# Kernel tuning notes

Hardware: AMD Instinct MI355X
Metric: run time of the kernel (lower is better)

## Reference

```python
import jax, jax.numpy as jnp
import numpy as np
from jax import lax

B, CIN, COUT, H, W, WDIM, K = 8, 256, 256, 64, 64, 512, 3
EPS = 1e-8
LRELU_SLOPE = 0.2


def setup_inputs() -> dict:
    key = jax.random.key(0)
    k_x, k_w, k_n, k_sw, k_cw = jax.random.split(key, 5)
    x = jax.random.normal(k_x, (B, CIN, H, W), dtype=jnp.float32)
    w = jax.random.normal(k_w, (B, WDIM), dtype=jnp.float32)
    noise = jax.random.normal(k_n, (B, 1, H, W), dtype=jnp.float32)
    # Equalized-LR params: stored ~N(0,1), scaled at use-time by 1/sqrt(fan_in)
    style_weight = jax.random.normal(k_sw, (CIN, WDIM), dtype=jnp.float32)
    style_bias = jnp.ones((CIN,), dtype=jnp.float32)  # StyleGAN style bias init = 1
    conv_weight = jax.random.normal(k_cw, (COUT, CIN, K, K), dtype=jnp.float32)
    noise_weight = jnp.zeros((COUT,), dtype=jnp.float32)  # NoiseInjection per-channel scale
    bias = jnp.zeros((COUT,), dtype=jnp.float32)
    return {"x": x, "w": w, "noise": noise, "style_weight": style_weight,
            "style_bias": style_bias, "conv_weight": conv_weight,
            "noise_weight": noise_weight, "bias": bias}


def reference(x, w, noise, style_weight, style_bias, conv_weight, noise_weight, bias):
    # EqualizedLinear: s = w @ (W * 1/sqrt(w_dim))^T + b  -> [B, CIN]
    s = jnp.einsum("bd,cd->bc", w, style_weight) * (1.0 / np.sqrt(WDIM)) + style_bias
    # Equalized conv weight scale
    wk = conv_weight * (1.0 / np.sqrt(CIN * K * K))  # [COUT, CIN, K, K]
    # Demodulation coefficient per (sample, out-channel):
    # demod = rsqrt(sum_{cin,kh,kw} (wk * s)^2 + eps)
    w2 = jnp.einsum("oikl,oikl->oi", wk, wk)               # [COUT, CIN]
    demod = lax.rsqrt(jnp.einsum("oi,bi->bo", w2, s * s) + EPS)  # [B, COUT]
    # Equivalent fused form: scale input per-channel, one shared conv, scale output
    xm = x * s[:, :, None, None]
    y = lax.conv_general_dilated(
        xm, wk, window_strides=(1, 1), padding="SAME",
        dimension_numbers=("NCHW", "OIHW", "NCHW"))
    y = y * demod[:, :, None, None]
    # NoiseInjection + bias + LeakyReLU(0.2)
    y = y + noise_weight[None, :, None, None] * noise + bias[None, :, None, None]
    return jnp.where(y >= 0, y, LRELU_SLOPE * y)
```

## Files before the change

### kernel.cpp

```cpp
#include <hip/hip_runtime.h>
#include <hip/hip_bf16.h>


typedef __attribute__((ext_vector_type(8))) short bf16x8;
typedef __attribute__((ext_vector_type(4))) float f32x4;

#define INV_SQRT_WDIM 0.04419417382415922f

__global__ __launch_bounds__(256)
void style_kernel(const float* __restrict__ w, const float* __restrict__ sw,
                  const float* __restrict__ sb, float* __restrict__ s) {
  const int b = blockIdx.x;
  const int c = threadIdx.x;
  float acc = 0.f;
#pragma unroll 8
  for (int d = 0; d < 512; ++d) acc += w[b * 512 + d] * sw[c * 512 + d];
  s[b * 256 + c] = acc * INV_SQRT_WDIM + sb[c];
}

__global__ __launch_bounds__(256)
void demod_kernel(const float* __restrict__ cw, const float* __restrict__ s,
                  float* __restrict__ demod) {
  const int o = blockIdx.x;
  const int i = threadIdx.x;
  float w2 = 0.f;
#pragma unroll
  for (int t = 0; t < 9; ++t) {
    float v = cw[(o * 256 + i) * 9 + t];
    w2 += v * v;
  }
  __shared__ float red[4];
  for (int b = 0; b < 8; ++b) {
    float sv = s[b * 256 + i];
    float val = w2 * sv * sv;
#pragma unroll
    for (int off = 32; off > 0; off >>= 1) val += __shfl_down(val, off);
    if ((i & 63) == 0) red[i >> 6] = val;
    __syncthreads();
    if (i == 0) {
      float tot = red[0] + red[1] + red[2] + red[3];
      demod[b * 256 + o] = rsqrtf(tot * (1.0f / 2304.0f) + 1e-8f);
    }
    __syncthreads();
  }
}

__global__ __launch_bounds__(256)
void wtrans_kernel(const float* __restrict__ cw, __hip_bfloat16* __restrict__ wt) {
  const int e = blockIdx.x * 256 + threadIdx.x;
  const int tap = e >> 16;
  const int o = (e >> 8) & 255;
  const int i = e & 255;
  wt[e] = __float2bfloat16(cw[(o * 256 + i) * 9 + tap] * (1.0f / 48.0f));
}

__global__ __launch_bounds__(256)
void xmod_kernel(const float* __restrict__ x, const float* __restrict__ s,
                 __hip_bfloat16* __restrict__ xt) {
  const int h = blockIdx.x;
  const int b = blockIdx.y;
  __shared__ __hip_bfloat16 tile[256 * 66];
  const int t = threadIdx.x;
  const int wl4 = (t & 15) * 4;
#pragma unroll 4
  for (int p = 0; p < 16; ++p) {
    const int i = p * 16 + (t >> 4);
    const float4 v = *(const float4*)&x[((b * 256 + i) * 64 + h) * 64 + wl4];
    const float sv = s[b * 256 + i];
    const int wsw = wl4 ^ (((i >> 3) & 7) << 3);
    unsigned lo = ((unsigned)__bfloat16_as_ushort(__float2bfloat16(v.y * sv)) << 16) |
                  (unsigned)__bfloat16_as_ushort(__float2bfloat16(v.x * sv));
    unsigned hi = ((unsigned)__bfloat16_as_ushort(__float2bfloat16(v.w * sv)) << 16) |
                  (unsigned)__bfloat16_as_ushort(__float2bfloat16(v.z * sv));
    *(unsigned*)&tile[i * 66 + wsw] = lo;
    *(unsigned*)&tile[i * 66 + wsw + 2] = hi;
  }
  __syncthreads();
#pragma unroll 2
  for (int p = 0; p < 8; ++p) {
    const int w = p * 8 + (t >> 5);
    const int c = t & 31;
    ushort out8[8];
#pragma unroll
    for (int j = 0; j < 8; ++j) {
      const int i = c * 8 + j;
      const int wsw = w ^ (((i >> 3) & 7) << 3);
      out8[j] = __bfloat16_as_ushort(tile[i * 66 + wsw]);
    }
    *(uint4*)&xt[((b * 64 + h) * 64 + w) * 256 + c * 8] = *(uint4*)out8;
  }
}

__global__ __launch_bounds__(256, 2)
void conv_mfma_kernel(const __hip_bfloat16* __restrict__ xt,
                      const __hip_bfloat16* __restrict__ wt,
                      const float* __restrict__ demod,
                      const float* __restrict__ noise,
                      const float* __restrict__ nw,
                      const float* __restrict__ bias,
                      float* __restrict__ out) {
  __shared__ __hip_bfloat16 xlds[6 * 64 * 32] __attribute__((aligned(16)));
  __shared__ __hip_bfloat16 wlds[9 * 64 * 32] __attribute__((aligned(16)));

  const int tid = threadIdx.x;
  const int lane = tid & 63;
  const int wv = tid >> 6;

  const int h0 = blockIdx.x * 4;
  const int oc0 = blockIdx.y * 64;
  const int b = blockIdx.z;

  const int abase = (lane & 15) * 32 + 8 * (lane >> 4);

  int boff[4][3];
  bool bok[4][3];
#pragma unroll
  for (int q = 0; q < 4; ++q)
#pragma unroll
    for (int tj = 0; tj < 3; ++tj) {
      int wx = q * 16 + (lane & 15) + tj - 1;
      bool ok = (unsigned)wx < 64u;
      int wc = ok ? wx : 0;
      boff[q][tj] = wc * 32 + 8 * (lane >> 4);
      bok[q][tj] = ok;
    }

  const f32x4 zero4 = {0.f, 0.f, 0.f, 0.f};
  const bf16x8 zerov = {0, 0, 0, 0, 0, 0, 0, 0};
  f32x4 acc[4][4];
#pragma unroll
  for (int m = 0; m < 4; ++m)
#pragma unroll
    for (int q = 0; q < 4; ++q) acc[m][q] = zero4;

  for (int cc = 0; cc < 8; ++cc) {
    const int c0 = cc * 32;
    __syncthreads();

#pragma unroll
    for (int k = 0; k < 6; ++k) {
      const int gX = tid + k * 256;
      const int r = gX >> 8;
      const int w = (gX >> 2) & 63;
      const int g = gX & 3;
      const int gr = h0 - 1 + r;
      uint4 v = make_uint4(0u, 0u, 0u, 0u);
      if ((unsigned)gr < 64u)
        v = *(const uint4*)&xt[((b * 64 + gr) * 64 + w) * 256 + c0 + 8 * g];
      *(uint4*)&xlds[gX * 8] = v;
    }
#pragma unroll
    for (int k = 0; k < 9; ++k) {
      const int gW = tid + k * 256;
      const int t9 = gW >> 8;
      const int o = (gW >> 2) & 63;
      const int g = gW & 3;
      uint4 v = *(const uint4*)&wt[t9 * 65536 + (oc0 + o) * 256 + c0 + 8 * g];
      *(uint4*)&wlds[gW * 8] = v;
    }
    __syncthreads();

#pragma unroll
    for (int ti = 0; ti < 3; ++ti) {
#pragma unroll
      for (int tj = 0; tj < 3; ++tj) {
        const int t = ti * 3 + tj;
        bf16x8 av[4];
#pragma unroll
        for (int m = 0; m < 4; ++m)
          av[m] = *(const bf16x8*)&wlds[t * 2048 + m * 512 + abase];
#pragma unroll
        for (int q = 0; q < 4; ++q) {
          bf16x8 bv = *(const bf16x8*)&xlds[(wv + ti) * 2048 + boff[q][tj]];
          if (!bok[q][tj]) bv = zerov;
#pragma unroll
          for (int m = 0; m < 4; ++m)
            acc[m][q] = __builtin_amdgcn_mfma_f32_16x16x32_bf16(av[m], bv, acc[m][q], 0, 0, 0);
        }
      }
    }
  }

  const int hrow = h0 + wv;
  float nzv[4];
#pragma unroll
  for (int q = 0; q < 4; ++q)
    nzv[q] = noise[b * 4096 + hrow * 64 + q * 16 + (lane & 15)];
#pragma unroll
  for (int m = 0; m < 4; ++m) {
#pragma unroll
    for (int reg = 0; reg < 4; ++reg) {
      const int oc = oc0 + m * 16 + (lane >> 4) * 4 + reg;
      const float dm = demod[b * 256 + oc];
      const float nwv = nw[oc];
      const float bvv = bias[oc];
#pragma unroll
      for (int q = 0; q < 4; ++q) {
        float v = acc[m][q][reg] * dm + nwv * nzv[q] + bvv;
        v = (v >= 0.f) ? v : 0.2f * v;
        out[((b * 256 + oc) * 64 + hrow) * 64 + q * 16 + (lane & 15)] = v;
      }
    }
  }
}

extern "C" void kernel_launch(void* const* d_in, const int* in_sizes, int n_in,
                              void* d_out, int out_size, void* d_ws, size_t ws_size,
                              hipStream_t stream) {
  const float* x     = (const float*)d_in[0];
  const float* w     = (const float*)d_in[1];
  const float* noise = (const float*)d_in[2];
  const float* sw    = (const float*)d_in[3];
  const float* sb    = (const float*)d_in[4];
  const float* cw    = (const float*)d_in[5];
  const float* nw    = (const float*)d_in[6];
  const float* bias  = (const float*)d_in[7];
  float* out = (float*)d_out;

  char* ws = (char*)d_ws;
  float* s            = (float*)(ws);
  float* demod        = (float*)(ws + 8192);
  __hip_bfloat16* wt  = (__hip_bfloat16*)(ws + 16384);
  __hip_bfloat16* xt  = (__hip_bfloat16*)(ws + 1196032);

  style_kernel<<<8, 256, 0, stream>>>(w, sw, sb, s);
  demod_kernel<<<256, 256, 0, stream>>>(cw, s, demod);
  wtrans_kernel<<<2304, 256, 0, stream>>>(cw, wt);
  xmod_kernel<<<dim3(64, 8), 256, 0, stream>>>(x, s, xt);
  conv_mfma_kernel<<<dim3(16, 4, 8), 256, 0, stream>>>(
      xt, wt, demod, noise, nw, bias, out);
}
```

Before: 163.3 us.

## Double-buffer input tiles via direct-to-LDS loads, read weights from global, fuse prep kernels

The conv kernel now stages the modulated input tile straight into LDS with global_load_lds, double-buffered so the next channel chunk loads while the current one computes. Weights are no longer staged in LDS. They are pre-laid out in MFMA fragment order and read directly from global, which frees LDS so occupancy can go to 3 blocks per SM. The style GEMV is parallelised over channels, and the demod and weight-transpose kernels are merged into one. The input layout gets an XOR slot swizzle, and a zero buffer covers out-of-range rows. The risks are higher latency from global weight reads inside the MFMA loop and register pressure at the new launch bound.

```diff
diff --git a/kernel.cpp b/kernel.cpp
--- a/kernel.cpp
+++ b/kernel.cpp
@@ -7,51 +7,75 @@
 
 #define INV_SQRT_WDIM 0.04419417382415922f
 
+__device__ __forceinline__ void gload_lds16(const void* g, void* l) {
+  __builtin_amdgcn_global_load_lds(
+      (const __attribute__((address_space(1))) void*)g,
+      (__attribute__((address_space(3))) void*)l, 16, 0, 0);
+}
+
 __global__ __launch_bounds__(256)
-void style_kernel(const float* __restrict__ w, const float* __restrict__ sw,
-                  const float* __restrict__ sb, float* __restrict__ s) {
-  const int b = blockIdx.x;
-  const int c = threadIdx.x;
-  float acc = 0.f;
-#pragma unroll 8
-  for (int d = 0; d < 512; ++d) acc += w[b * 512 + d] * sw[c * 512 + d];
-  s[b * 256 + c] = acc * INV_SQRT_WDIM + sb[c];
+void style2_kernel(const float* __restrict__ w, const float* __restrict__ sw,
+                   const float* __restrict__ sb, float* __restrict__ s) {
+  const int c = blockIdx.x, t = threadIdx.x;
+  const int lane = t & 63, wvi = t >> 6;
+  const float2 swv = *(const float2*)&sw[c * 512 + t * 2];
+  __shared__ float red[4][8];
+  float acc[8];
+#pragma unroll
+  for (int b = 0; b < 8; ++b) {
+    const float2 wv2 = *(const float2*)&w[b * 512 + t * 2];
+    acc[b] = swv.x * wv2.x + swv.y * wv2.y;
+  }
+#pragma unroll
+  for (int b = 0; b < 8; ++b)
+#pragma unroll
+    for (int off = 32; off > 0; off >>= 1) acc[b] += __shfl_down(acc[b], off);
+  if (lane == 0)
+#pragma unroll
+    for (int b = 0; b < 8; ++b) red[wvi][b] = acc[b];
+  __syncthreads();
+  if (t < 8) {
+    float tot = red[0][t] + red[1][t] + red[2][t] + red[3][t];
+    s[t * 256 + c] = tot * INV_SQRT_WDIM + sb[c];
+  }
 }
 
 __global__ __launch_bounds__(256)
-void demod_kernel(const float* __restrict__ cw, const float* __restrict__ s,
-                  float* __restrict__ demod) {
-  const int o = blockIdx.x;
-  const int i = threadIdx.x;
+void wdm_kernel(const float* __restrict__ cw, const float* __restrict__ s,
+                __hip_bfloat16* __restrict__ wt2, float* __restrict__ demod) {
+  const int o = blockIdx.x, i = threadIdx.x;
+  const int lane = i & 63, wvi = i >> 6;
+  float v[9];
   float w2 = 0.f;
 #pragma unroll
   for (int t = 0; t < 9; ++t) {
-    float v = cw[(o * 256 + i) * 9 + t];
-    w2 += v * v;
-  }
-  __shared__ float red[4];
+    v[t] = cw[(o * 256 + i) * 9 + t];
+    w2 += v[t] * v[t];
+  }
+  const int wbase = (i >> 5) * 8192 + (o >> 4) * 512 + ((i >> 3) & 3) * 128 +
+                    (o & 15) * 8 + (i & 7);
+#pragma unroll
+  for (int t = 0; t < 9; ++t)
+    wt2[t * 65536 + wbase] = __float2bfloat16(v[t] * (1.0f / 48.0f));
+  __shared__ float red[4][8];
+  float pv[8];
+#pragma unroll
   for (int b = 0; b < 8; ++b) {
-    float sv = s[b * 256 + i];
-    float val = w2 * sv * sv;
-#pragma unroll
-    for (int off = 32; off > 0; off >>= 1) val += __shfl_down(val, off);
-    if ((i & 63) == 0) red[i >> 6] = val;
-    __syncthreads();
-    if (i == 0) {
-      float tot = red[0] + red[1] + red[2] + red[3];
-      demod[b * 256 + o] = rsqrtf(tot * (1.0f / 2304.0f) + 1e-8f);
-    }
-    __syncthreads();
-  }
-}
-
-__global__ __launch_bounds__(256)
-void wtrans_kernel(const float* __restrict__ cw, __hip_bfloat16* __restrict__ wt) {
-  const int e = blockIdx.x * 256 + threadIdx.x;
-  const int tap = e >> 16;
-  const int o = (e >> 8) & 255;
-  const int i = e & 255;
-  wt[e] = __float2bfloat16(cw[(o * 256 + i) * 9 + tap] * (1.0f / 48.0f));
+    const float sv = s[b * 256 + i];
+    pv[b] = w2 * sv * sv;
+  }
+#pragma unroll
+  for (int b = 0; b < 8; ++b)
+#pragma unroll
+    for (int off = 32; off > 0; off >>= 1) pv[b] += __shfl_down(pv[b], off);
+  if (lane == 0)
+#pragma unroll
+    for (int b = 0; b < 8; ++b) red[wvi][b] = pv[b];
+  __syncthreads();
+  if (i < 8) {
+    float tot = red[0][i] + red[1][i] + red[2][i] + red[3][i];
+    demod[i * 256 + o] = rsqrtf(tot * (1.0f / 2304.0f) + 1e-8f);
+  }
 }
 
 __global__ __launch_bounds__(256)
@@ -87,20 +111,22 @@
       const int wsw = w ^ (((i >> 3) & 7) << 3);
       out8[j] = __bfloat16_as_ushort(tile[i * 66 + wsw]);
     }
-    *(uint4*)&xt[((b * 64 + h) * 64 + w) * 256 + c * 8] = *(uint4*)out8;
-  }
-}
-
-__global__ __launch_bounds__(256, 2)
+    const int slot = (c & 3) ^ ((w >> 1) & 3);
+    *(uint4*)&xt[((b * 64 + h) * 64 + w) * 256 + (c >> 2) * 32 + slot * 8] =
+        *(uint4*)out8;
+  }
+}
+
+__global__ __launch_bounds__(256, 3)
 void conv_mfma_kernel(const __hip_bfloat16* __restrict__ xt,
-                      const __hip_bfloat16* __restrict__ wt,
+                      const __hip_bfloat16* __restrict__ wt2,
                       const float* __restrict__ demod,
                       const float* __restrict__ noise,
                       const float* __restrict__ nw,
                       const float* __restrict__ bias,
+                      const __hip_bfloat16* __restrict__ zbuf,
                       float* __restrict__ out) {
-  __shared__ __hip_bfloat16 xlds[6 * 64 * 32] __attribute__((aligned(16)));
-  __shared__ __hip_bfloat16 wlds[9 * 64 * 32] __attribute__((aligned(16)));
+  __shared__ __hip_bfloat16 xlds[2][12288] __attribute__((aligned(16)));
 
   const int tid = threadIdx.x;
   const int lane = tid & 63;
@@ -110,7 +136,8 @@
   const int oc0 = blockIdx.y * 64;
   const int b = blockIdx.z;
 
-  const int abase = (lane & 15) * 32 + 8 * (lane >> 4);
+  const int aoff = (lane >> 4) * 128 + (lane & 15) * 8;
+  const int o16b = oc0 >> 4;
 
   int boff[4][3];
   bool bok[4][3];
@@ -121,7 +148,8 @@
       int wx = q * 16 + (lane & 15) + tj - 1;
       bool ok = (unsigned)wx < 64u;
       int wc = ok ? wx : 0;
-      boff[q][tj] = wc * 32 + 8 * (lane >> 4);
+      int slot = (lane >> 4) ^ ((wc >> 1) & 3);
+      boff[q][tj] = wc * 32 + slot * 8;
       bok[q][tj] = ok;
     }
 
@@ -133,33 +161,28 @@
 #pragma unroll
     for (int q = 0; q < 4; ++q) acc[m][q] = zero4;
 
+  auto stage = [&](int buf, int scc) {
+#pragma unroll
+    for (int k = 0; k < 6; ++k) {
+      const int ch = wv * 6 + k;
+      const int r = ch >> 2;
+      const int wseg = ch & 3;
+      const int gr = h0 - 1 + r;
+      const __hip_bfloat16* src =
+          ((unsigned)gr < 64u)
+              ? xt + ((b * 64 + gr) * 64 + wseg * 16 + (lane >> 2)) * 256 +
+                    scc * 32 + (lane & 3) * 8
+              : zbuf;
+      gload_lds16(src, &xlds[buf][ch * 512]);
+    }
+  };
+
+  stage(0, 0);
+  __syncthreads();
+
   for (int cc = 0; cc < 8; ++cc) {
-    const int c0 = cc * 32;
-    __syncthreads();
-
-#pragma unroll
-    for (int k = 0; k < 6; ++k) {
-      const int gX = tid + k * 256;
-      const int r = gX >> 8;
-      const int w = (gX >> 2) & 63;
-      const int g = gX & 3;
-      const int gr = h0 - 1 + r;
-      uint4 v = make_uint4(0u, 0u, 0u, 0u);
-      if ((unsigned)gr < 64u)
-        v = *(const uint4*)&xt[((b * 64 + gr) * 64 + w) * 256 + c0 + 8 * g];
-      *(uint4*)&xlds[gX * 8] = v;
-    }
-#pragma unroll
-    for (int k = 0; k < 9; ++k) {
-      const int gW = tid + k * 256;
-      const int t9 = gW >> 8;
-      const int o = (gW >> 2) & 63;
-      const int g = gW & 3;
-      uint4 v = *(const uint4*)&wt[t9 * 65536 + (oc0 + o) * 256 + c0 + 8 * g];
-      *(uint4*)&wlds[gW * 8] = v;
-    }
-    __syncthreads();
-
+    const int cur = cc & 1;
+    if (cc < 7) stage(cur ^ 1, cc + 1);
 #pragma unroll
     for (int ti = 0; ti < 3; ++ti) {
 #pragma unroll
@@ -168,17 +191,20 @@
         bf16x8 av[4];
 #pragma unroll
         for (int m = 0; m < 4; ++m)
-          av[m] = *(const bf16x8*)&wlds[t * 2048 + m * 512 + abase];
+          av[m] = *(const bf16x8*)&wt2[t * 65536 + cc * 8192 +
+                                       (o16b + m) * 512 + aoff];
 #pragma unroll
         for (int q = 0; q < 4; ++q) {
-          bf16x8 bv = *(const bf16x8*)&xlds[(wv + ti) * 2048 + boff[q][tj]];
+          bf16x8 bv = *(const bf16x8*)&xlds[cur][(wv + ti) * 2048 + boff[q][tj]];
           if (!bok[q][tj]) bv = zerov;
 #pragma unroll
           for (int m = 0; m < 4; ++m)
-            acc[m][q] = __builtin_amdgcn_mfma_f32_16x16x32_bf16(av[m], bv, acc[m][q], 0, 0, 0);
+            acc[m][q] = __builtin_amdgcn_mfma_f32_16x16x32_bf16(av[m], bv,
+                                                                acc[m][q], 0, 0, 0);
         }
       }
     }
+    __syncthreads();
   }
 
   const int hrow = h0 + wv;
@@ -220,13 +246,14 @@
   char* ws = (char*)d_ws;
   float* s            = (float*)(ws);
   float* demod        = (float*)(ws + 8192);
-  __hip_bfloat16* wt  = (__hip_bfloat16*)(ws + 16384);
-  __hip_bfloat16* xt  = (__hip_bfloat16*)(ws + 1196032);
-
-  style_kernel<<<8, 256, 0, stream>>>(w, sw, sb, s);
-  demod_kernel<<<256, 256, 0, stream>>>(cw, s, demod);
-  wtrans_kernel<<<2304, 256, 0, stream>>>(cw, wt);
+  __hip_bfloat16* zbuf = (__hip_bfloat16*)(ws + 16384);
+  __hip_bfloat16* wt2 = (__hip_bfloat16*)(ws + 17408);
+  __hip_bfloat16* xt  = (__hip_bfloat16*)(ws + 1197056);
+
+  hipMemsetAsync(zbuf, 0, 1024, stream);
+  style2_kernel<<<256, 256, 0, stream>>>(w, sw, sb, s);
+  wdm_kernel<<<256, 256, 0, stream>>>(cw, s, wt2, demod);
   xmod_kernel<<<dim3(64, 8), 256, 0, stream>>>(x, s, xt);
   conv_mfma_kernel<<<dim3(16, 4, 8), 256, 0, stream>>>(
-      xt, wt, demod, noise, nw, bias, out);
-}
+      xt, wt2, demod, noise, nw, bias, zbuf, out);
+}
```

Result: faster. 154.0 us (-5.7%).
